# Performance work log

Measured on AMD Instinct MI355X. Metric: run time of the kernel, lower is better.

The kernel has to match this reference:

```python
import itertools
import jax, jax.numpy as jnp
import numpy as np

THR = 0.2  # success_threshold (non-trainable constant)
V = 2      # num_total_variables
U_IDX, B_IDX = 1, 2  # rule_idxs for arities [0,1,2]


def _perm_indices(num_objects: int, v: int):
    """Static permutation index tables (numpy, shapes are compile-time)."""
    perm_idxs = np.array(list(itertools.permutations(range(num_objects), v)))  # [P, V]
    bidx = np.stack(np.nonzero(1 - np.eye(v))).T.reshape(v, v - 1, 2)          # [V, V-1, 2]
    pb = perm_idxs[:, bidx]                                                     # [P, V, V-1, 2]
    shift = (pb[..., 1] > pb[..., 0]).astype(np.int64)
    perm_bidxs = np.stack([pb[..., 0], pb[..., 1] - shift], axis=-1)            # off-diagonal compact idx
    return jnp.asarray(perm_idxs), jnp.asarray(perm_bidxs)


def setup_inputs() -> dict:
    key = jax.random.key(0)
    k1, k2, k3, k4, k5 = jax.random.split(key, 5)
    B, O, P0, P1, P2, C = 16, 64, 128, 128, 128, 8
    num_in = P0 + V * P1 + V * (V - 1) * P2  # 640
    return {
        "nullary": jax.random.normal(k1, (B, P0), dtype=jnp.float32),
        "unary": jax.random.normal(k2, (B, O, P1), dtype=jnp.float32),
        "binary": jax.random.normal(k3, (B, O, O - 1, P2), dtype=jnp.float32),
        "and_kernel": 0.01 * jax.random.normal(k4, (3, C, num_in), dtype=jnp.float32),
        "or_kernel": 0.01 * jax.random.normal(k5, (3, C), dtype=jnp.float32),
    }


def _forward(nullary, unary, binary, and_kernel, or_kernel):
    B, O, _ = unary.shape
    perm_idxs, perm_bidxs = _perm_indices(O, V)
    P = perm_idxs.shape[0]  # O*(O-1) for V=2
    thr = jnp.float32(THR)

    # permutation gathers -> flatten_concat with batch_dims=2
    pn = jnp.broadcast_to(nullary[:, None], (B, P, nullary.shape[-1]))          # [B,P,P0]
    pu = unary[:, perm_idxs].reshape(B, P, -1)                                   # [B,P,V*P1]
    pb = binary[:, perm_bidxs[..., 0], perm_bidxs[..., 1]].reshape(B, P, -1)     # [B,P,V*(V-1)*P2]
    x = jnp.concatenate([pn, pu, pb], axis=-1)                                   # [B,P,num_in]

    # AND stage: multiply-sum + bias + tanh (einsum == sum(in_tensor * and_kernel, -1))
    and_bias = thr - jnp.sum(jnp.square(and_kernel), -1) * jnp.tanh(thr)         # [A,C]
    conj = jnp.tanh(jnp.einsum('bpi,aci->bpac', x, and_kernel) + and_bias)       # [B,P,A,C]

    A, C = and_kernel.shape[0], and_kernel.shape[1]
    # OR max-reduce over unused permutation dims
    null_r = jnp.max(conj[:, :, :U_IDX, :], axis=1)                              # [B,n0,C]
    un_r = conj[:, :, U_IDX:B_IDX, :].reshape(B, O, P // O, B_IDX - U_IDX, C).max(axis=2)
    bi_r = conj[:, :, B_IDX:, :].reshape(B, O, O - 1, P // (O * (O - 1)), A - B_IDX, C).max(axis=3)

    def or_stage(c, k):
        bias = jnp.sum(jnp.square(k), -1) * jnp.tanh(thr) - thr                  # [n_rules]
        return jnp.einsum('...rc,rc->...r', c, k) + bias

    return (or_stage(null_r, or_kernel[:U_IDX]),
            or_stage(un_r, or_kernel[U_IDX:B_IDX]),
            or_stage(bi_r, or_kernel[B_IDX:]))


def reference(nullary, unary, binary, and_kernel, or_kernel):
    # outputs: nullary [B,1], unary [B,O,1], binary [B,O,O-1,1]
    return _forward(nullary, unary, binary, and_kernel, or_kernel)
```

## Files before the change

kernel.cpp:

```cpp
#include <hip/hip_runtime.h>

#define THR_F     0.2f
#define TANH_THR  0.19737532f

__device__ __forceinline__ float fast_tanh(float x) {
    x = fminf(10.f, fmaxf(-10.f, x));
    float e = __expf(2.f * x);
    return (e - 1.f) * __builtin_amdgcn_rcpf(e + 1.f);
}

__device__ __forceinline__ unsigned fkey(float f) {
    unsigned u = __float_as_uint(f);
    return (u & 0x80000000u) ? ~u : (u | 0x80000000u);
}
__device__ __forceinline__ float fdecode(unsigned u) {
    return __uint_as_float((u & 0x80000000u) ? (u & 0x7FFFFFFFu) : ~u);
}

__global__ __launch_bounds__(64) void prep_kernel(
    const float* __restrict__ nullary,
    const float* __restrict__ andk,
    float* __restrict__ Wb,
    float* __restrict__ WuT,
    float* __restrict__ base,
    unsigned* __restrict__ zzero)
{
    const int bid = blockIdx.x;
    const int t   = threadIdx.x;
    if (bid < 384) {
        const int b = bid / 24, n = bid % 24;
        const float* w  = andk + n * 640;
        const float* nu = nullary + b * 128;
        float s = 0.f;
        #pragma unroll
        for (int i = 0; i < 10; ++i) { float v = w[t + i * 64]; s = fmaf(v, v, s); }
        float d = fmaf(nu[t], w[t], 0.f);
        d = fmaf(nu[t + 64], w[t + 64], d);
        #pragma unroll
        for (int m = 32; m; m >>= 1) {
            s += __shfl_xor(s, m, 64);
            d += __shfl_xor(d, m, 64);
        }
        if (t == 0) base[bid] = d + THR_F - s * TANH_THR;
    } else if (bid < 480) {
        const int i = (bid - 384) * 64 + t;
        {
            const int k = i / 48, n = i % 48;
            const int ac  = (n < 24) ? n : n - 24;
            const int col = (n < 24) ? 384 : 512;
            Wb[i] = andk[ac * 640 + col + k];
        }
        {
            const int n = i / 128, k = i % 128;
            const int ac  = (n < 24) ? n : n - 24;
            const int col = (n < 24) ? 128 : 256;
            WuT[i] = andk[ac * 640 + col + k];
        }
    } else {
        const int idx = (bid - 480) * 64 + t;
        if (idx < 8320) zzero[idx] = 0u;
    }
}

__global__ __launch_bounds__(128) void fused_kernel(
    const float* __restrict__ unary,
    const float* __restrict__ binary,
    const float* __restrict__ Wb,
    const float* __restrict__ WuT,
    const float* __restrict__ base,
    const float* __restrict__ ork,
    unsigned* __restrict__ max0,
    unsigned* __restrict__ slots1,
    float* __restrict__ out)
{
    __shared__ float proj2[48][65];
    __shared__ float upro[48][13];

    const int bid = blockIdx.x;
    const int b   = bid >> 6;
    const int tl  = bid & 63;
    const int t   = threadIdx.x;

    int gi, gj, H;
    bool diag;
    if (tl < 8) { diag = true; gi = gj = tl; H = 0; }
    else {
        diag = false;
        int t8 = tl - 8;
        H = t8 & 1;
        int pr = t8 >> 1;
        int i = 0;
        while (pr >= 7 - i) { pr -= 7 - i; ++i; }
        gi = i; gj = i + 1 + pr;
    }
    const int I0 = gi * 8, J0 = gj * 8;

    {
        const int r = t & 63;
        const int h = __builtin_amdgcn_readfirstlane(t >> 6);
        int o, op, jv;
        if (diag) {
            const int oi = r >> 3, oj = r & 7;
            o = I0 + oi; op = I0 + oj;
            jv = op - ((oj > oi) ? 1 : 0);
        } else if (r < 32) {
            const int oi = H * 4 + (r >> 3), oj = r & 7;
            o = I0 + oi; op = J0 + oj;
            jv = op - 1;
        } else {
            const int rr = r - 32;
            const int oi = rr >> 2, oj = H * 4 + (rr & 3);
            o = J0 + oi; op = I0 + oj;
            jv = op;
        }
        jv = min(jv, 62);
        const float* __restrict__ src = binary + ((size_t)(b * 64 + o) * 63 + jv) * 128;
        const float* __restrict__ W   = Wb + h * 24;

        float acc[24];
        #pragma unroll
        for (int n = 0; n < 24; ++n) acc[n] = 0.f;
        const float4* rp = (const float4*)src;
        #pragma unroll 4
        for (int k4 = 0; k4 < 32; ++k4) {
            float4 a = rp[k4];
            const float* wk = W + k4 * 4 * 48;
            #pragma unroll
            for (int q = 0; q < 4; ++q) {
                float av = (q == 0) ? a.x : (q == 1) ? a.y : (q == 2) ? a.z : a.w;
                const float* w = wk + q * 48;
                #pragma unroll
                for (int n = 0; n < 24; ++n) acc[n] = fmaf(av, w[n], acc[n]);
            }
        }
        #pragma unroll
        for (int n = 0; n < 24; ++n) proj2[h * 24 + n][r] = acc[n];
    }

    {
        const int nObj = diag ? 8 : 12;
        if (t < nObj * 8) {
            const int u = t >> 3, nb = t & 7, n0 = nb * 6;
            const int obj = diag ? (I0 + u)
                                 : (u < 4 ? (I0 + H * 4 + u) : (J0 + u - 4));
            const float4* su = (const float4*)(unary + (size_t)(b * 64 + obj) * 128);
            float a6[6];
            #pragma unroll
            for (int j = 0; j < 6; ++j) a6[j] = 0.f;
            #pragma unroll 4
            for (int k4 = 0; k4 < 32; ++k4) {
                float4 a = su[k4];
                #pragma unroll
                for (int j = 0; j < 6; ++j) {
                    float4 w = ((const float4*)(WuT + (n0 + j) * 128))[k4];
                    a6[j] = fmaf(a.x, w.x, fmaf(a.y, w.y, fmaf(a.z, w.z, fmaf(a.w, w.w, a6[j]))));
                }
            }
            #pragma unroll
            for (int j = 0; j < 6; ++j) upro[n0 + j][u] = a6[j];
        }
    }
    __syncthreads();

    const int p = t & 63;
    int o0, o1, r0, r1, u0, u1, j01;
    bool valid;
    if (diag) {
        const int qi = p >> 3, qj = p & 7;
        valid = (qi != qj);
        o0 = I0 + qi; o1 = I0 + qj;
        r0 = p; r1 = qj * 8 + qi;
        u0 = qi; u1 = qj;
        j01 = o1 - ((qj > qi) ? 1 : 0);
    } else if (p < 32) {
        const int qi = p >> 3, qj = p & 7;
        valid = true;
        o0 = I0 + H * 4 + qi; o1 = J0 + qj;
        r0 = p; r1 = 32 + qj * 4 + qi;
        u0 = qi; u1 = 4 + qj;
        j01 = o1 - 1;
    } else {
        const int pp = p - 32;
        const int qi = pp >> 2, qj = pp & 3;
        valid = true;
        o0 = J0 + qi; o1 = I0 + H * 4 + qj;
        r0 = 32 + qi * 4 + qj; r1 = qj * 8 + qi;
        u0 = 4 + qi; u1 = qj;
        j01 = o1;
    }
    const float* pb = base + b * 24;

    if (t >= 64) {
        float v = 0.f, b2 = 0.f;
        #pragma unroll
        for (int c = 0; c < 8; ++c) {
            const int ch = 16 + c;
            float x = pb[ch] + upro[ch][u0] + upro[24 + ch][u1]
                    + proj2[ch][r0] + proj2[24 + ch][r1];
            x = fast_tanh(x);
            float k = ork[16 + c];
            v  = fmaf(x, k, v);
            b2 = fmaf(k, k, b2);
        }
        if (valid) out[16 + 1024 + (b * 64 + o0) * 63 + j01] = v + b2 * TANH_THR - THR_F;
        return;
    }

    float th[16];
    #pragma unroll
    for (int c = 0; c < 16; ++c) {
        float x = pb[c] + upro[c][u0] + upro[24 + c][u1]
                + proj2[c][r0] + proj2[24 + c][r1];
        th[c] = fast_tanh(x);
    }
    if (!valid) {
        #pragma unroll
        for (int c = 0; c < 16; ++c) th[c] = -2.f;
    }

    #pragma unroll
    for (int c = 0; c < 8; ++c) {
        float v = th[c];
        #pragma unroll
        for (int m = 32; m; m >>= 1) v = fmaxf(v, __shfl_xor(v, m, 64));
        th[c] = v;
    }
    if (p == 0) {
        #pragma unroll
        for (int c = 0; c < 8; ++c)
            atomicMax(&max0[b * 8 + c], fkey(th[c]));
    }

    float m4[8], m8[8];
    #pragma unroll
    for (int c = 0; c < 8; ++c) {
        float v = th[8 + c];
        v = fmaxf(v, __shfl_xor(v, 1, 64));
        v = fmaxf(v, __shfl_xor(v, 2, 64));
        m4[c] = v;
        m8[c] = fmaxf(v, __shfl_xor(v, 4, 64));
    }
    const bool emit8 = (diag || p < 32) && ((p & 7) == 0);
    const bool emit4 = (!diag && p >= 32) && ((p & 3) == 0);
    if (emit8) {
        #pragma unroll
        for (int c = 0; c < 8; ++c)
            atomicMax(&slots1[(b * 64 + o0) * 8 + c], fkey(m8[c]));
    }
    if (emit4) {
        #pragma unroll
        for (int c = 0; c < 8; ++c)
            atomicMax(&slots1[(b * 64 + o0) * 8 + c], fkey(m4[c]));
    }
}

__global__ __launch_bounds__(256) void finalize_kernel(
    const unsigned* __restrict__ max0,
    const unsigned* __restrict__ slots1,
    const float* __restrict__ ork,
    float* __restrict__ out)
{
    const int bid = blockIdx.x, t = threadIdx.x;
    if (bid < 4) {
        const int i = bid * 256 + t;
        float v = 0.f, bb = 0.f;
        #pragma unroll
        for (int c = 0; c < 8; ++c) {
            float m = fdecode(slots1[i * 8 + c]);
            float k = ork[8 + c];
            v  = fmaf(m, k, v);
            bb = fmaf(k, k, bb);
        }
        out[16 + i] = v + bb * TANH_THR - THR_F;
    } else if (t < 16) {
        float v = 0.f, bb = 0.f;
        #pragma unroll
        for (int c = 0; c < 8; ++c) {
            float m = fdecode(max0[t * 8 + c]);
            float k = ork[c];
            v  = fmaf(m, k, v);
            bb = fmaf(k, k, bb);
        }
        out[t] = v + bb * TANH_THR - THR_F;
    }
}

extern "C" void kernel_launch(void* const* d_in, const int* in_sizes, int n_in,
                              void* d_out, int out_size, void* d_ws, size_t ws_size,
                              hipStream_t stream)
{
    const float* nullary = (const float*)d_in[0];
    const float* unary   = (const float*)d_in[1];
    const float* binary  = (const float*)d_in[2];
    const float* andk    = (const float*)d_in[3];
    const float* ork     = (const float*)d_in[4];
    float* out = (float*)d_out;

    float* ws = (float*)d_ws;
    float*    Wb     = ws;
    float*    WuT    = ws + 6144;
    float*    base   = ws + 12288;
    unsigned* max0   = (unsigned*)(ws + 12672);
    unsigned* slots1 = max0 + 128;

    prep_kernel<<<610, 64, 0, stream>>>(nullary, andk, Wb, WuT, base, max0);
    fused_kernel<<<1024, 128, 0, stream>>>(unary, binary, Wb, WuT, base, ork,
                                           max0, slots1, out);
    finalize_kernel<<<5, 256, 0, stream>>>(max0, slots1, ork, out);
}
```

Baseline: 153.4 us.

## Precompute unary projections once in a separate kernel instead of per block

```diff
diff --git a/kernel.cpp b/kernel.cpp
--- a/kernel.cpp
+++ b/kernel.cpp
@@ -21,7 +21,7 @@
     const float* __restrict__ nullary,
     const float* __restrict__ andk,
     float* __restrict__ Wb,
-    float* __restrict__ WuT,
+    float* __restrict__ Wu,
     float* __restrict__ base,
     unsigned* __restrict__ zzero)
 {
@@ -44,29 +44,57 @@
         if (t == 0) base[bid] = d + THR_F - s * TANH_THR;
     } else if (bid < 480) {
         const int i = (bid - 384) * 64 + t;
-        {
-            const int k = i / 48, n = i % 48;
-            const int ac  = (n < 24) ? n : n - 24;
-            const int col = (n < 24) ? 384 : 512;
-            Wb[i] = andk[ac * 640 + col + k];
-        }
-        {
-            const int n = i / 128, k = i % 128;
-            const int ac  = (n < 24) ? n : n - 24;
-            const int col = (n < 24) ? 128 : 256;
-            WuT[i] = andk[ac * 640 + col + k];
-        }
+        const int k = i / 48, n = i % 48;
+        const int ac   = (n < 24) ? n : n - 24;
+        const int colb = (n < 24) ? 384 : 512;
+        const int colu = (n < 24) ? 128 : 256;
+        Wb[i] = andk[ac * 640 + colb + k];
+        Wu[i] = andk[ac * 640 + colu + k];
     } else {
         const int idx = (bid - 480) * 64 + t;
         if (idx < 8320) zzero[idx] = 0u;
     }
 }
 
+__global__ __launch_bounds__(256) void uproj_kernel(
+    const float* __restrict__ unary,
+    const float* __restrict__ Wu,
+    float* __restrict__ U)
+{
+    const int wave = __builtin_amdgcn_readfirstlane((int)(threadIdx.x >> 6));
+    const int lane = threadIdx.x & 63;
+    const int row  = blockIdx.x * 64 + lane;
+    const float* __restrict__ W   = Wu + wave * 12;
+    const float* __restrict__ src = unary + (size_t)row * 128;
+
+    float acc[12];
+    #pragma unroll
+    for (int n = 0; n < 12; ++n) acc[n] = 0.f;
+
+    const float4* rp = (const float4*)src;
+    #pragma unroll 8
+    for (int k4 = 0; k4 < 32; ++k4) {
+        float4 a = rp[k4];
+        const float* wk = W + k4 * 4 * 48;
+        #pragma unroll
+        for (int q = 0; q < 4; ++q) {
+            float av = (q == 0) ? a.x : (q == 1) ? a.y : (q == 2) ? a.z : a.w;
+            const float* w = wk + q * 48;
+            #pragma unroll
+            for (int n = 0; n < 12; ++n) acc[n] = fmaf(av, w[n], acc[n]);
+        }
+    }
+
+    float4* d4 = (float4*)(U + (size_t)row * 48 + wave * 12);
+    #pragma unroll
+    for (int i = 0; i < 3; ++i)
+        d4[i] = make_float4(acc[i*4+0], acc[i*4+1], acc[i*4+2], acc[i*4+3]);
+}
+
 __global__ __launch_bounds__(128) void fused_kernel(
-    const float* __restrict__ unary,
+    const float* __restrict__ U,
     const float* __restrict__ binary,
     const float* __restrict__ Wb,
-    const float* __restrict__ WuT,
     const float* __restrict__ base,
     const float* __restrict__ ork,
     unsigned* __restrict__ max0,
@@ -74,7 +102,7 @@
     float* __restrict__ out)
 {
     __shared__ float proj2[48][65];
-    __shared__ float upro[48][13];
+    __shared__ float upro[12][52];
 
     const int bid = blockIdx.x;
     const int b   = bid >> 6;
@@ -94,6 +122,15 @@
         gi = i; gj = i + 1 + pr;
     }
     const int I0 = gi * 8, J0 = gj * 8;
+    const int nObj = diag ? 8 : 12;
+
+    for (int i = t; i < nObj * 12; i += 128) {
+        const int u = i / 12, q = i % 12;
+        const int obj = diag ? (I0 + u)
+                             : (u < 4 ? (I0 + H * 4 + u) : (J0 + u - 4));
+        float4 v = ((const float4*)(U + (size_t)(b * 64 + obj) * 48))[q];
+        *((float4*)&upro[u][q * 4]) = v;
+    }
 
     {
         const int r = t & 63;
@@ -135,30 +172,6 @@
         }
         #pragma unroll
         for (int n = 0; n < 24; ++n) proj2[h * 24 + n][r] = acc[n];
-    }
-
-    {
-        const int nObj = diag ? 8 : 12;
-        if (t < nObj * 8) {
-            const int u = t >> 3, nb = t & 7, n0 = nb * 6;
-            const int obj = diag ? (I0 + u)
-                                 : (u < 4 ? (I0 + H * 4 + u) : (J0 + u - 4));
-            const float4* su = (const float4*)(unary + (size_t)(b * 64 + obj) * 128);
-            float a6[6];
-            #pragma unroll
-            for (int j = 0; j < 6; ++j) a6[j] = 0.f;
-            #pragma unroll 4
-            for (int k4 = 0; k4 < 32; ++k4) {
-                float4 a = su[k4];
-                #pragma unroll
-                for (int j = 0; j < 6; ++j) {
-                    float4 w = ((const float4*)(WuT + (n0 + j) * 128))[k4];
-                    a6[j] = fmaf(a.x, w.x, fmaf(a.y, w.y, fmaf(a.z, w.z, fmaf(a.w, w.w, a6[j]))));
-                }
-            }
-            #pragma unroll
-            for (int j = 0; j < 6; ++j) upro[n0 + j][u] = a6[j];
-        }
     }
     __syncthreads();
 
@@ -195,7 +208,7 @@
         #pragma unroll
         for (int c = 0; c < 8; ++c) {
             const int ch = 16 + c;
-            float x = pb[ch] + upro[ch][u0] + upro[24 + ch][u1]
+            float x = pb[ch] + upro[u0][ch] + upro[u1][24 + ch]
                     + proj2[ch][r0] + proj2[24 + ch][r1];
             x = fast_tanh(x);
             float k = ork[16 + c];
@@ -209,7 +222,7 @@
     float th[16];
     #pragma unroll
     for (int c = 0; c < 16; ++c) {
-        float x = pb[c] + upro[c][u0] + upro[24 + c][u1]
+        float x = pb[c] + upro[u0][c] + upro[u1][24 + c]
                 + proj2[c][r0] + proj2[24 + c][r1];
         th[c] = fast_tanh(x);
     }
@@ -298,13 +311,15 @@
 
     float* ws = (float*)d_ws;
     float*    Wb     = ws;
-    float*    WuT    = ws + 6144;
+    float*    Wu     = ws + 6144;
     float*    base   = ws + 12288;
-    unsigned* max0   = (unsigned*)(ws + 12672);
+    float*    U      = ws + 12672;
+    unsigned* max0   = (unsigned*)(ws + 61824);
     unsigned* slots1 = max0 + 128;
 
-    prep_kernel<<<610, 64, 0, stream>>>(nullary, andk, Wb, WuT, base, max0);
-    fused_kernel<<<1024, 128, 0, stream>>>(unary, binary, Wb, WuT, base, ork,
+    prep_kernel<<<610, 64, 0, stream>>>(nullary, andk, Wb, Wu, base, max0);
+    uproj_kernel<<<16, 256, 0, stream>>>(unary, Wu, U);
+    fused_kernel<<<1024, 128, 0, stream>>>(U, binary, Wb, base, ork,
                                            max0, slots1, out);
     finalize_kernel<<<5, 256, 0, stream>>>(max0, slots1, ork, out);
 }
```

New measurement: 135.1 us. 1.14x faster.
